# Kernel optimization log

Hardware: AMD Instinct MI355X
Metric: run time of the kernel (lower is better)

Reference implementation:

```python
import jax, jax.numpy as jnp
import numpy as np

V, D, L, H, T, B = 128, 256, 2, 4, 4096, 8
DK, DV = 128, 256           # key_dim=0.5*D, value_dim=1.0*D (fla GLA defaults)
HK, HV = DK // H, DV // H   # 32, 64
GLN = 16.0                  # gate_logit_normalizer
CH = 64                     # chunk size
EPS = 1e-5

def layernorm(x, w, b):
    mu = x.mean(-1, keepdims=True)
    var = ((x - mu) ** 2).mean(-1, keepdims=True)
    return (x - mu) * jax.lax.rsqrt(var + EPS) * w + b

def gla_chunk(q, k, v, gk, scale):
    # q,k,gk: [B,T,H,HK], v: [B,T,H,HV]; gk are per-key log decay gates (<=0)
    B_, T_, H_, dk = q.shape
    dv = v.shape[-1]
    N = T_ // CH
    def rs(x):
        d = x.shape[-1]
        return x.reshape(B_, N, CH, H_, d).transpose(0, 3, 1, 2, 4)  # [B,H,N,C,d]
    q, k, v, gk = rs(q), rs(k), rs(v), rs(gk)
    b = jnp.cumsum(gk, axis=3)                       # inclusive within-chunk cumlog decay
    q_s = q * jnp.exp(b) * scale
    k_i = k * jnp.exp(-b)                            # for intra-chunk attention
    k_e = k * jnp.exp(b[..., -1:, :] - b)            # decayed to chunk end, for state update
    mask = jnp.tril(jnp.ones((CH, CH), bool))
    att = jnp.einsum('bhncd,bhnmd->bhncm', q_s, k_i)
    att = jnp.where(mask, att, 0.0)
    o_intra = jnp.einsum('bhncm,bhnmd->bhncd', att, v)
    g_last = jnp.exp(b[..., -1, :])                  # [B,H,N,dk] full-chunk decay
    kv = jnp.einsum('bhncd,bhnce->bhnde', k_e, v)    # [B,H,N,dk,dv]
    def step(S, inp):
        qc, gl, kvc = inp
        o = jnp.einsum('bhcd,bhde->bhce', qc, S)
        return S * gl[..., None] + kvc, o
    S0 = jnp.zeros((B_, H_, dk, dv), q.dtype)
    xs = (jnp.moveaxis(q_s, 2, 0), jnp.moveaxis(g_last, 2, 0), jnp.moveaxis(kv, 2, 0))
    _, o_inter = jax.lax.scan(step, S0, xs)
    o = o_intra + jnp.moveaxis(o_inter, 0, 2)        # [B,H,N,C,dv]
    return o.transpose(0, 2, 3, 1, 4).reshape(B_, T_, H_, dv)

def gla_attn(x, wq, wk, wv, wg, gk_w1, gk_w2, gk_b2, gnorm_w, wo):
    B_, T_, _ = x.shape
    q = (x @ wq).reshape(B_, T_, H, HK)
    k = (x @ wk).reshape(B_, T_, H, HK)
    v = (x @ wv).reshape(B_, T_, H, HV)
    gk = jax.nn.log_sigmoid(x @ gk_w1 @ gk_w2 + gk_b2) / GLN
    gk = gk.reshape(B_, T_, H, HK)
    o = gla_chunk(q, k, v, gk, HK ** -0.5)           # [B,T,H,HV]
    g = (x @ wg).reshape(B_, T_, H, HV)
    rms = jax.lax.rsqrt((o * o).mean(-1, keepdims=True) + EPS)
    o = o * rms * gnorm_w * (g * jax.nn.sigmoid(g))  # FusedRMSNormSwishGate
    return o.reshape(B_, T_, DV) @ wo

def setup_inputs() -> dict:
    key = jax.random.key(0)
    ks = jax.random.split(key, 16)
    s = 0.02
    return {
        'tokens': jax.random.randint(ks[0], (B, T), 0, V),
        'embed': jax.random.normal(ks[1], (V, D)) * s,
        'ln_w': jnp.ones((L, D)), 'ln_b': jnp.zeros((L, D)),
        'wq': jax.random.normal(ks[2], (L, D, DK)) * s,
        'wk': jax.random.normal(ks[3], (L, D, DK)) * s,
        'wv': jax.random.normal(ks[4], (L, D, DV)) * s,
        'wg': jax.random.normal(ks[5], (L, D, DV)) * s,
        'gk_w1': jax.random.normal(ks[6], (L, D, 16)) * s,
        'gk_w2': jax.random.normal(ks[7], (L, 16, DK)) * s,
        'gk_b2': jnp.zeros((L, DK)),
        'gnorm_w': jnp.ones((L, HV)),
        'wo': jax.random.normal(ks[8], (L, DV, D)) * s,
        'mlp_w1': jax.random.normal(ks[9], (L, D, 2 * D)) * s,
        'mlp_b1': jnp.zeros((L, 2 * D)),
        'mlp_w2': jax.random.normal(ks[10], (L, 2 * D, D)) * s,
        'mlp_b2': jnp.zeros((L, D)),
        'head_w': jax.random.normal(ks[11], (D, V)) * s,
        'head_b': jnp.zeros((V,)),
    }

def reference(tokens, embed, ln_w, ln_b, wq, wk, wv, wg, gk_w1, gk_w2, gk_b2,
              gnorm_w, wo, mlp_w1, mlp_b1, mlp_w2, mlp_b2, head_w, head_b):
    x = embed[tokens]
    for i in range(L):
        h = layernorm(x, ln_w[i], ln_b[i])
        x = x + gla_attn(h, wq[i], wk[i], wv[i], wg[i], gk_w1[i], gk_w2[i],
                         gk_b2[i], gnorm_w[i], wo[i])
        h = layernorm(x, ln_w[i], ln_b[i])
        x = x + jax.nn.gelu(h @ mlp_w1[i] + mlp_b1[i], approximate=False) @ mlp_w2[i] + mlp_b2[i]
    return x @ head_w + head_b
```

## Files before the change

kernel.cpp:

```cpp
#include <hip/hip_runtime.h>
#include <hip/hip_bf16.h>
#include <math.h>

namespace {

constexpr int Bq = 8, Tq = 4096, Dq = 256, Lq = 2, Hq = 4;
constexpr int DKq = 128, DVq = 256, HKq = 32, HVq = 64;
constexpr int Nq = Tq / 64;
constexpr int Mq = Bq * Tq;
constexpr int SQ = 896;
constexpr float SCALEq = 0.17677669529663688f;
constexpr int WL = 1114112;

typedef __hip_bfloat16 bf16;
typedef __attribute__((ext_vector_type(8))) short bf16x8;
typedef __attribute__((ext_vector_type(4))) float f32x4;

__device__ __forceinline__ float b2f(bf16 x) { return __bfloat162float(x); }

__device__ __forceinline__ bf16x8 ld8(const bf16* p) { return *(const bf16x8*)p; }
__device__ __forceinline__ bf16x8 ld8(const float* p) {
  const float4* q4 = (const float4*)p;
  float4 a = q4[0], b = q4[1];
  float v[8] = {a.x, a.y, a.z, a.w, b.x, b.y, b.z, b.w};
  bf16x8 r;
#pragma unroll
  for (int i = 0; i < 8; i++) r[i] = __builtin_bit_cast(short, __float2bfloat16(v[i]));
  return r;
}

__device__ __forceinline__ int swzk(int k, int row) {
  return (k & ~63) | ((((k >> 3) & 7) ^ (row & 7)) << 3) | (k & 7);
}

__device__ __forceinline__ size_t fidx(int n, int k, int K) {
  int ct = n >> 7, nt = (n >> 4) & 7, lr = n & 15;
  int k0 = k >> 6, kk = (k >> 5) & 1, lg = (k >> 3) & 3, e = k & 7;
  int fi = ((ct * (K >> 6) + k0) * 2 + kk) * 8 + nt;
  return (size_t)fi * 512 + (lg * 16 + lr) * 8 + e;
}

__device__ __forceinline__ void wsplit2(float v, bf16* hi, bf16* lo) {
  bf16 h = __float2bfloat16(v);
  *hi = h; *lo = __float2bfloat16(v - b2f(h));
}

__global__ void k_wprep(const float* __restrict__ wq, const float* __restrict__ wk,
                        const float* __restrict__ wv, const float* __restrict__ wg,
                        const float* __restrict__ g1, const float* __restrict__ g2,
                        const float* __restrict__ wo, const float* __restrict__ m1,
                        const float* __restrict__ m2, const float* __restrict__ hw,
                        bf16* __restrict__ Wt) {
  int g = blockIdx.x * 256 + threadIdx.x;
  if (g >= 2 * 540672 + 32768) return;
  if (g < 2 * 540672) {
    int l = g / 540672, r = g % 540672;
    bf16* dst = Wt + (size_t)l * WL;
    if (r < 196608) {
      int k, nf; float v;
      if (r < 32768)       { int r2 = r;          k = r2 >> 7; nf = (r2 & 127);       v = wq[l*32768 + r2]; }
      else if (r < 65536)  { int r2 = r - 32768;  k = r2 >> 7; nf = 128 + (r2 & 127); v = wk[l*32768 + r2]; }
      else if (r < 131072) { int r2 = r - 65536;  k = r2 >> 8; nf = 256 + (r2 & 255); v = wv[l*65536 + r2]; }
      else                 { int r2 = r - 131072; k = r2 >> 8; nf = 512 + (r2 & 255); v = wg[l*65536 + r2]; }
      size_t fo = fidx(nf, k, 256);
      wsplit2(v, &dst[fo], &dst[229376 + fo]);
    } else if (r < 212992) {
      int r2 = r - 196608; int k = r2 >> 7, n = r2 & 127;
      float v = 0.f;
#pragma unroll
      for (int i = 0; i < 16; i++) v += g1[l*4096 + k*16 + i] * g2[l*2048 + i*128 + n];
      size_t fo = fidx(768 + n, k, 256);
      wsplit2(v, &dst[fo], &dst[229376 + fo]);
    } else if (r < 278528) {
      int r2 = r - 212992; int k = r2 >> 8, n = r2 & 255;
      size_t fo = fidx(n, k, 256);
      wsplit2(wo[l*65536 + r2], &dst[458752 + fo], &dst[524288 + fo]);
    } else if (r < 409600) {
      int r2 = r - 278528; int k = r2 >> 9, n = r2 & 511;
      size_t fo = fidx(n, k, 256);
      wsplit2(m1[l*131072 + r2], &dst[589824 + fo], &dst[720896 + fo]);
    } else {
      int r2 = r - 409600; int k = r2 >> 8, n = r2 & 255;
      size_t fo = fidx(n, k, 512);
      wsplit2(m2[l*131072 + r2], &dst[851968 + fo], &dst[983040 + fo]);
    }
  } else {
    int r2 = g - 2 * 540672; int k = r2 >> 7, n = r2 & 127;
    size_t fo = fidx(n, k, 256);
    wsplit2(hw[r2], &Wt[2228224 + fo], &Wt[2228224 + 32768 + fo]);
  }
}

__global__ void k_embed(const int* __restrict__ tok, const float* __restrict__ emb,
                        float* __restrict__ x) {
  int row = blockIdx.x, i = threadIdx.x;
  x[(size_t)row * Dq + i] = emb[(size_t)tok[row] * Dq + i];
}

__global__ void k_ln(const float* __restrict__ x, const float* __restrict__ w,
                     const float* __restrict__ bb, bf16* __restrict__ h) {
  int row = blockIdx.x, i = threadIdx.x;
  float v = x[(size_t)row * Dq + i];
  float s = v, s2 = v * v;
#pragma unroll
  for (int o = 32; o > 0; o >>= 1) { s += __shfl_down(s, o, 64); s2 += __shfl_down(s2, o, 64); }
  __shared__ float rs[4], rs2[4];
  if ((i & 63) == 0) { rs[i >> 6] = s; rs2[i >> 6] = s2; }
  __syncthreads();
  float sum = rs[0] + rs[1] + rs[2] + rs[3];
  float sum2 = rs2[0] + rs2[1] + rs2[2] + rs2[3];
  float mu = sum * (1.f / Dq);
  float var = fmaxf(sum2 * (1.f / Dq) - mu * mu, 0.f);
  float r = rsqrtf(var + 1e-5f);
  h[(size_t)row * Dq + i] = __float2bfloat16((v - mu) * r * w[i] + bb[i]);
}

template <typename AT, typename OT, int EPI, bool BIAS, bool ACC, bool GATEA>
__global__ __launch_bounds__(256, 2) void k_mgemm8(const AT* __restrict__ A, int lda,
                                                   const bf16* __restrict__ Whf,
                                                   const bf16* __restrict__ Wlf,
                                                   const float* __restrict__ bias,
                                                   OT* __restrict__ C, int ldc, int K,
                                                   const bf16* __restrict__ GQ,
                                                   const float* __restrict__ gnw) {
  __shared__ __attribute__((aligned(16))) bf16 At[128 * 256];
  int tid = threadIdx.x;
  int lane = tid & 63, wave = tid >> 6;
  int lr = lane & 15, lg = lane >> 4;
  int wm = (wave >> 1) * 64, wn = (wave & 1) * 64;
  int row0 = blockIdx.x * 128;
  int ct = blockIdx.y, nk = K >> 6;
  f32x4 acc[4][4];
#pragma unroll
  for (int m = 0; m < 4; m++)
#pragma unroll
    for (int n = 0; n < 4; n++) acc[m][n] = (f32x4){0.f, 0.f, 0.f, 0.f};

  for (int kc = 0; kc < K; kc += 256) {
    if (kc) __syncthreads();
#pragma unroll
    for (int p = 0; p < 16; p++) {
      int cix = p * 256 + tid, r = cix >> 5, j = (cix & 31) * 8;
      bf16x8 v = ld8(A + (size_t)(row0 + r) * lda + kc + j);
      if constexpr (GATEA) {
        float o[8]; float s = 0.f;
#pragma unroll
        for (int i = 0; i < 8; i++) { o[i] = b2f(__builtin_bit_cast(bf16, (short)v[i])); s += o[i] * o[i]; }
        s += __shfl_xor(s, 1, 64); s += __shfl_xor(s, 2, 64); s += __shfl_xor(s, 4, 64);
        float rr = rsqrtf(s * (1.f / 64.f) + 1e-5f);
        bf16x8 g8 = *(const bf16x8*)(GQ + (size_t)(row0 + r) * SQ + 512 + j);
#pragma unroll
        for (int i = 0; i < 8; i++) {
          float g = b2f(__builtin_bit_cast(bf16, (short)g8[i]));
          float sw = g / (1.f + expf(-g));
          v[i] = __builtin_bit_cast(short, __float2bfloat16(o[i] * rr * gnw[(j + i) & 63] * sw));
        }
      }
      *(bf16x8*)&At[r * 256 + swzk(j, r)] = v;
    }
    __syncthreads();
#pragma unroll
    for (int k0l = 0; k0l < 256; k0l += 64) {
      int k0 = kc + k0l;
      int k0i = k0 >> 6;
#pragma unroll
      for (int kk = 0; kk < 64; kk += 32) {
        int fb = ((ct * nk + k0i) * 2 + (kk >> 5)) * 8 + (wn >> 4);
        const bf16* bhp = Whf + (size_t)fb * 512 + lane * 8;
        const bf16* blp = Wlf + (size_t)fb * 512 + lane * 8;
        bf16x8 af[4], bh4[4], bl4[4];
#pragma unroll
        for (int n = 0; n < 4; n++) {
          bh4[n] = *(const bf16x8*)(bhp + n * 512);
          bl4[n] = *(const bf16x8*)(blp + n * 512);
        }
#pragma unroll
        for (int m = 0; m < 4; m++) {
          int ar = wm + m * 16 + lr;
          af[m] = *(bf16x8*)&At[ar * 256 + swzk(k0l + kk + lg * 8, ar)];
        }
#pragma unroll
        for (int m = 0; m < 4; m++)
#pragma unroll
          for (int n = 0; n < 4; n++) {
            acc[m][n] = __builtin_amdgcn_mfma_f32_16x16x32_bf16(af[m], bh4[n], acc[m][n], 0, 0, 0);
            acc[m][n] = __builtin_amdgcn_mfma_f32_16x16x32_bf16(af[m], bl4[n], acc[m][n], 0, 0, 0);
          }
      }
    }
  }
#pragma unroll
  for (int m = 0; m < 4; m++) {
#pragma unroll
    for (int n = 0; n < 4; n++) {
      int col = ct * 128 + wn + n * 16 + lr;
      int rowb = row0 + wm + m * 16 + lg * 4;
      float bv = BIAS ? bias[col] : 0.f;
#pragma unroll
      for (int j = 0; j < 4; j++) {
        float v = acc[m][n][j] + bv;
        if (EPI == 2) v = 0.5f * v * (1.f + erff(v * 0.70710678118654752f));
        if (EPI == 3 && col >= 768) {
          float t = v + bias[col - 768];
          v = (fminf(t, 0.f) - log1pf(expf(-fabsf(t)))) * (1.f / 16.f);
        }
        size_t oi = (size_t)(rowb + j) * ldc + col;
        if constexpr (ACC) C[oi] += v;
        else if constexpr (sizeof(OT) == 2) C[oi] = __float2bfloat16(v);
        else C[oi] = v;
      }
    }
  }
}

__global__ __launch_bounds__(256) void k_intra(bf16* QKVG,
                                               bf16* __restrict__ O,
                                               bf16* __restrict__ KVt,
                                               float* __restrict__ GL) {
  int blk = blockIdx.x;
  int n = blk & 63, h = (blk >> 6) & 3, b = blk >> 8;
  __shared__ __attribute__((aligned(16))) char smem[47488];
  float* bshT = (float*)smem;
  bf16*  kvS  = (bf16*)smem;
  float* glv  = (float*)(smem + 8448);
  bf16*  vT   = (bf16*)(smem + 8576);
  bf16*  kiAH = (bf16*)(smem + 17792);
  bf16*  kiAL = (bf16*)(smem + 22400);
  bf16*  qsH  = (bf16*)(smem + 27008);
  bf16*  qsL  = (bf16*)(smem + 32128);
  bf16*  kiBH = (bf16*)(smem + 37248);
  bf16*  kiBL = (bf16*)(smem + 42368);
  bf16*  aH   = (bf16*)(smem + 27008);
  bf16*  aL   = (bf16*)(smem + 36224);
  int tid = threadIdx.x;
  int lane = tid & 63, wave = tid >> 6;
  int lr = lane & 15, lg = lane >> 4;
  size_t tbase = (size_t)b * Tq + n * 64;
  int bh = b * Hq + h;

  {
    int c = tid >> 2, dc = (tid & 3) * 8;
    bf16x8 g8 = *(const bf16x8*)(QKVG + (tbase + c) * SQ + 768 + h * HKq + dc);
#pragma unroll
    for (int i = 0; i < 8; i++) bshT[(dc + i) * 66 + c] = b2f(__builtin_bit_cast(bf16, (short)g8[i]));
  }
  __syncthreads();
#pragma unroll
  for (int dd = 0; dd < 8; dd++) {
    int d = wave * 8 + dd;
    float v = bshT[d * 66 + lane];
#pragma unroll
    for (int o = 1; o < 64; o <<= 1) {
      float t = __shfl_up(v, (unsigned)o, 64);
      if (lane >= o) v += t;
    }
    bshT[d * 66 + lane] = v;
  }
  __syncthreads();
  if (tid < 32) {
    float g = expf(bshT[tid * 66 + 63]);
    glv[tid] = g;
    GL[(size_t)(bh * Nq + n) * 32 + tid] = g;
  }
  {
    int c = tid >> 2, dc = (tid & 3) * 8;
    size_t qoff = (tbase + c) * SQ + h * HKq + dc;
    bf16x8 q8 = *(const bf16x8*)(QKVG + qoff);
    bf16x8 k8 = *(const bf16x8*)(QKVG + qoff + 128);
    bf16x8 qh8, ql8, kh8, kl8;
#pragma unroll
    for (int i = 0; i < 8; i++) {
      float bv = bshT[(dc + i) * 66 + c];
      float qv = b2f(__builtin_bit_cast(bf16, (short)q8[i])) * expf(bv) * SCALEq;
      float kv = b2f(__builtin_bit_cast(bf16, (short)k8[i])) * expf(-bv);
      bf16 qh = __float2bfloat16(qv); bf16 ql = __float2bfloat16(qv - b2f(qh));
      bf16 kh = __float2bfloat16(kv); bf16 kl = __float2bfloat16(kv - b2f(kh));
      qh8[i] = __builtin_bit_cast(short, qh); ql8[i] = __builtin_bit_cast(short, ql);
      kh8[i] = __builtin_bit_cast(short, kh); kl8[i] = __builtin_bit_cast(short, kl);
      kiAH[(dc + i) * 72 + c] = kh; kiAL[(dc + i) * 72 + c] = kl;
    }
    *(bf16x8*)&qsH[c * 40 + dc] = qh8;
    *(bf16x8*)&qsL[c * 40 + dc] = ql8;
    *(bf16x8*)&kiBH[c * 40 + dc] = kh8;
    *(bf16x8*)&kiBL[c * 40 + dc] = kl8;
    *(bf16x8*)(QKVG + qoff) = qh8;
  }
#pragma unroll
  for (int p = 0; p < 2; p++) {
    int idx = p * 256 + tid;
    int c = idx & 63, ec = (idx >> 6) * 8;
    bf16x8 v8 = *(const bf16x8*)(QKVG + (tbase + c) * SQ + 256 + h * HVq + ec);
#pragma unroll
    for (int i = 0; i < 8; i++) vT[(ec + i) * 72 + c] = __builtin_bit_cast(bf16, (short)v8[i]);
  }
  __syncthreads();
  f32x4 accq[4];
#pragma unroll
  for (int t = 0; t < 4; t++) accq[t] = (f32x4){0.f, 0.f, 0.f, 0.f};
  {
    bf16x8 afh = *(bf16x8*)&qsH[(wave * 16 + lr) * 40 + lg * 8];
    bf16x8 afl = *(bf16x8*)&qsL[(wave * 16 + lr) * 40 + lg * 8];
#pragma unroll
    for (int t = 0; t < 4; t++) {
      bf16x8 bh = *(bf16x8*)&kiBH[(t * 16 + lr) * 40 + lg * 8];
      bf16x8 bl = *(bf16x8*)&kiBL[(t * 16 + lr) * 40 + lg * 8];
      accq[t] = __builtin_amdgcn_mfma_f32_16x16x32_bf16(afh, bh, accq[t], 0, 0, 0);
      accq[t] = __builtin_amdgcn_mfma_f32_16x16x32_bf16(afh, bl, accq[t], 0, 0, 0);
      accq[t] = __builtin_amdgcn_mfma_f32_16x16x32_bf16(afl, bh, accq[t], 0, 0, 0);
    }
  }
  __syncthreads();
#pragma unroll
  for (int t = 0; t < 4; t++)
#pragma unroll
    for (int j = 0; j < 4; j++) {
      int row = wave * 16 + lg * 4 + j;
      int col = t * 16 + lr;
      float v = (col <= row) ? accq[t][j] : 0.f;
      bf16 hi = __float2bfloat16(v);
      aH[row * 72 + col] = hi;
      aL[row * 72 + col] = __float2bfloat16(v - b2f(hi));
    }
  __syncthreads();
  f32x4 acco[4];
#pragma unroll
  for (int t = 0; t < 4; t++) acco[t] = (f32x4){0.f, 0.f, 0.f, 0.f};
#pragma unroll
  for (int ks = 0; ks < 2; ks++) {
    bf16x8 ah = *(bf16x8*)&aH[(wave * 16 + lr) * 72 + ks * 32 + lg * 8];
    bf16x8 al = *(bf16x8*)&aL[(wave * 16 + lr) * 72 + ks * 32 + lg * 8];
#pragma unroll
    for (int t = 0; t < 4; t++) {
      bf16x8 bfv = *(bf16x8*)&vT[(t * 16 + lr) * 72 + ks * 32 + lg * 8];
      acco[t] = __builtin_amdgcn_mfma_f32_16x16x32_bf16(ah, bfv, acco[t], 0, 0, 0);
      acco[t] = __builtin_amdgcn_mfma_f32_16x16x32_bf16(al, bfv, acco[t], 0, 0, 0);
    }
  }
#pragma unroll
  for (int t = 0; t < 4; t++)
#pragma unroll
    for (int j = 0; j < 4; j++) {
      int row = wave * 16 + lg * 4 + j, e = t * 16 + lr;
      O[(tbase + row) * DVq + h * HVq + e] = __float2bfloat16(acco[t][j]);
    }
  f32x4 acck[2];
  acck[0] = (f32x4){0.f, 0.f, 0.f, 0.f};
  acck[1] = (f32x4){0.f, 0.f, 0.f, 0.f};
#pragma unroll
  for (int ks = 0; ks < 2; ks++) {
    bf16x8 akh = *(bf16x8*)&kiAH[((wave >> 1) * 16 + lr) * 72 + ks * 32 + lg * 8];
    bf16x8 akl = *(bf16x8*)&kiAL[((wave >> 1) * 16 + lr) * 72 + ks * 32 + lg * 8];
#pragma unroll
    for (int t = 0; t < 2; t++) {
      bf16x8 bfv = *(bf16x8*)&vT[(((wave & 1) * 2 + t) * 16 + lr) * 72 + ks * 32 + lg * 8];
      acck[t] = __builtin_amdgcn_mfma_f32_16x16x32_bf16(akh, bfv, acck[t], 0, 0, 0);
      acck[t] = __builtin_amdgcn_mfma_f32_16x16x32_bf16(akl, bfv, acck[t], 0, 0, 0);
    }
  }
#pragma unroll
  for (int t = 0; t < 2; t++)
#pragma unroll
    for (int j = 0; j < 4; j++) {
      int d = (wave >> 1) * 16 + lg * 4 + j;
      int e = ((wave & 1) * 2 + t) * 16 + lr;
      kvS[d * 72 + e] = __float2bfloat16(acck[t][j] * glv[d]);
    }
  __syncthreads();
  size_t kbase = (size_t)(bh * Nq + n) * 2048;
  {
    int d = tid >> 3, cc = (tid & 7) * 8;
    *(bf16x8*)&KVt[kbase + d * 64 + cc] = *(bf16x8*)&kvS[d * 72 + cc];
  }
}

__global__ __launch_bounds__(256) void k_inter(const bf16* __restrict__ QKVG,
                                               const float* __restrict__ GL,
                                               const bf16* __restrict__ KVt,
                                               bf16* __restrict__ O) {
  int blk = blockIdx.x;
  int es = blk & 7, h = (blk >> 3) & 3, b = blk >> 5;
  int e0 = es * 8;
  __shared__ __attribute__((aligned(16))) bf16 kvl[64 * 32 * 8];
  __shared__ float gl[64 * 32];
  __shared__ float S[64 * 32 * 8];
  int tid = threadIdx.x;
  int bh = b * Hq + h;
  const float* glp = GL + (size_t)bh * Nq * 32;
#pragma unroll
  for (int p = 0; p < 8; p++) { int i = p * 256 + tid; gl[i] = glp[i]; }
  const bf16* kvp = KVt + (size_t)bh * Nq * 2048 + e0;
#pragma unroll
  for (int p = 0; p < 8; p++) {
    int c8 = p * 256 + tid;
    *(bf16x8*)&kvl[c8 * 8] = *(const bf16x8*)(kvp + (size_t)(c8 >> 5) * 2048 + (size_t)(c8 & 31) * 64);
  }
  __syncthreads();
  {
    int pe = tid & 7, pd = tid >> 3;
    float s = 0.f;
    for (int n = 0; n < 64; n++) {
      S[(n * 32 + pd) * 8 + pe] = s;
      s = s * gl[n * 32 + pd] + b2f(kvl[(n * 32 + pd) * 8 + pe]);
    }
  }
  __syncthreads();
  int c = tid >> 2, ep = tid & 3;
  for (int n = 0; n < 64; n++) {
    size_t tbase = (size_t)b * Tq + n * 64;
    const bf16* qp = QKVG + (tbase + c) * SQ + h * HKq;
    const float* Sp = &S[n * 256];
    float a0 = 0.f, a1 = 0.f;
#pragma unroll
    for (int j = 0; j < 4; j++) {
      bf16x8 q8 = *(const bf16x8*)(qp + j * 8);
#pragma unroll
      for (int i = 0; i < 8; i++) {
        float qf = b2f(__builtin_bit_cast(bf16, (short)q8[i]));
        int d = j * 8 + i;
        a0 += qf * Sp[d * 8 + ep];
        a1 += qf * Sp[d * 8 + ep + 4];
      }
    }
    size_t oi = (tbase + c) * DVq + h * HVq + e0 + ep;
    O[oi] = __float2bfloat16(b2f(O[oi]) + a0);
    O[oi + 4] = __float2bfloat16(b2f(O[oi + 4]) + a1);
  }
}

}

extern "C" void kernel_launch(void* const* d_in, const int* in_sizes, int n_in,
                              void* d_out, int out_size, void* d_ws, size_t ws_size,
                              hipStream_t stream) {
  const int*   tok  = (const int*)d_in[0];
  const float* emb  = (const float*)d_in[1];
  const float* ln_w = (const float*)d_in[2];
  const float* ln_b = (const float*)d_in[3];
  const float* wq   = (const float*)d_in[4];
  const float* wk   = (const float*)d_in[5];
  const float* wv   = (const float*)d_in[6];
  const float* wg   = (const float*)d_in[7];
  const float* gkw1 = (const float*)d_in[8];
  const float* gkw2 = (const float*)d_in[9];
  const float* gkb2 = (const float*)d_in[10];
  const float* gnw  = (const float*)d_in[11];
  const float* wo   = (const float*)d_in[12];
  const float* mw1  = (const float*)d_in[13];
  const float* mb1  = (const float*)d_in[14];
  const float* mw2  = (const float*)d_in[15];
  const float* mb2  = (const float*)d_in[16];
  const float* hw   = (const float*)d_in[17];
  const float* hb   = (const float*)d_in[18];

  if (ws_size < 134217728u) return;
  char* w = (char*)d_ws;
  float* X    = (float*)w;
  bf16*  Ob   = (bf16*)(w + 33554432);
  bf16*  Hbf  = Ob;
  bf16*  QKVG = (bf16*)(w + 50331648);
  bf16*  KVt  = (bf16*)(w + 109051904);
  float* GLb  = (float*)(w + 117440512);
  bf16*  Wt   = (bf16*)(w + 117702656);
  bf16*  MLPH = QKVG;

  dim3 blk(256);
  k_wprep<<<4353, blk, 0, stream>>>(wq, wk, wv, wg, gkw1, gkw2, wo, mw1, mw2, hw, Wt);
  k_embed<<<Mq, blk, 0, stream>>>(tok, emb, X);

  for (int l = 0; l < Lq; l++) {
    const bf16* Wl = Wt + (size_t)l * WL;
    k_ln<<<Mq, blk, 0, stream>>>(X, ln_w + l * Dq, ln_b + l * Dq, Hbf);
    k_mgemm8<bf16, bf16, 3, false, false, false><<<dim3(256, 7), blk, 0, stream>>>(Hbf, 256, Wl, Wl + 229376, gkb2 + l * DKq, QKVG, SQ, 256, nullptr, nullptr);
    k_intra<<<Bq * Hq * Nq, blk, 0, stream>>>(QKVG, Ob, KVt, GLb);
    k_inter<<<Bq * Hq * 8, blk, 0, stream>>>(QKVG, GLb, KVt, Ob);
    k_mgemm8<bf16, float, 0, false, true, true><<<dim3(256, 2), blk, 0, stream>>>(Ob, 256, Wl + 458752, Wl + 524288, nullptr, X, 256, 256, QKVG, gnw + l * HVq);
    k_ln<<<Mq, blk, 0, stream>>>(X, ln_w + l * Dq, ln_b + l * Dq, Hbf);
    k_mgemm8<bf16, bf16, 2, true, false, false><<<dim3(256, 4), blk, 0, stream>>>(Hbf, 256, Wl + 589824, Wl + 720896, mb1 + l * 2 * Dq, MLPH, 512, 256, nullptr, nullptr);
    k_mgemm8<bf16, float, 0, true, true, false><<<dim3(256, 2), blk, 0, stream>>>(MLPH, 512, Wl + 851968, Wl + 983040, mb2 + l * Dq, X, 256, 512, nullptr, nullptr);
  }
  k_mgemm8<float, float, 0, true, false, false><<<dim3(256, 1), blk, 0, stream>>>(X, 256, Wt + 2228224, Wt + 2228224 + 32768, hb, (float*)d_out, 128, 256, nullptr, nullptr);
}
```

Baseline: 701.2 us.

## Shrink GEMM A-tile to 64-wide K slices and vectorize layernorm/embed rows

The GEMM now stages A in 64-column K slices instead of 256, cutting shared memory from 64KB to 16KB per block and raising launch bounds to 4 blocks per CU. The cost is an extra barrier per 64-wide slice and less work between barriers. Layernorm and embedding now process 8 rows per block, with each 32-lane group handling one row through float4 loads and bf16x8 stores. This removes the cross-wave shared-memory reduction and lowers the block count.

```diff
diff --git a/kernel.cpp b/kernel.cpp
--- a/kernel.cpp
+++ b/kernel.cpp
@@ -93,37 +93,44 @@
 
 __global__ void k_embed(const int* __restrict__ tok, const float* __restrict__ emb,
                         float* __restrict__ x) {
-  int row = blockIdx.x, i = threadIdx.x;
-  x[(size_t)row * Dq + i] = emb[(size_t)tok[row] * Dq + i];
+  int row = blockIdx.x * 8 + (threadIdx.x >> 5);
+  int j = (threadIdx.x & 31) * 8;
+  const float4* s = (const float4*)(emb + (size_t)tok[row] * Dq + j);
+  float4* d = (float4*)(x + (size_t)row * Dq + j);
+  d[0] = s[0]; d[1] = s[1];
 }
 
 __global__ void k_ln(const float* __restrict__ x, const float* __restrict__ w,
                      const float* __restrict__ bb, bf16* __restrict__ h) {
-  int row = blockIdx.x, i = threadIdx.x;
-  float v = x[(size_t)row * Dq + i];
-  float s = v, s2 = v * v;
-#pragma unroll
-  for (int o = 32; o > 0; o >>= 1) { s += __shfl_down(s, o, 64); s2 += __shfl_down(s2, o, 64); }
-  __shared__ float rs[4], rs2[4];
-  if ((i & 63) == 0) { rs[i >> 6] = s; rs2[i >> 6] = s2; }
-  __syncthreads();
-  float sum = rs[0] + rs[1] + rs[2] + rs[3];
-  float sum2 = rs2[0] + rs2[1] + rs2[2] + rs2[3];
-  float mu = sum * (1.f / Dq);
-  float var = fmaxf(sum2 * (1.f / Dq) - mu * mu, 0.f);
+  int row = blockIdx.x * 8 + (threadIdx.x >> 5);
+  int j = (threadIdx.x & 31) * 8;
+  const float4* xp = (const float4*)(x + (size_t)row * Dq + j);
+  float4 a = xp[0], b4 = xp[1];
+  float v[8] = {a.x, a.y, a.z, a.w, b4.x, b4.y, b4.z, b4.w};
+  float s = 0.f, s2 = 0.f;
+#pragma unroll
+  for (int i = 0; i < 8; i++) { s += v[i]; s2 += v[i] * v[i]; }
+#pragma unroll
+  for (int o = 16; o > 0; o >>= 1) { s += __shfl_xor(s, o, 64); s2 += __shfl_xor(s2, o, 64); }
+  float mu = s * (1.f / Dq);
+  float var = fmaxf(s2 * (1.f / Dq) - mu * mu, 0.f);
   float r = rsqrtf(var + 1e-5f);
-  h[(size_t)row * Dq + i] = __float2bfloat16((v - mu) * r * w[i] + bb[i]);
+  bf16x8 o8;
+#pragma unroll
+  for (int i = 0; i < 8; i++)
+    o8[i] = __builtin_bit_cast(short, __float2bfloat16((v[i] - mu) * r * w[j + i] + bb[j + i]));
+  *(bf16x8*)(h + (size_t)row * Dq + j) = o8;
 }
 
 template <typename AT, typename OT, int EPI, bool BIAS, bool ACC, bool GATEA>
-__global__ __launch_bounds__(256, 2) void k_mgemm8(const AT* __restrict__ A, int lda,
+__global__ __launch_bounds__(256, 4) void k_mgemm7(const AT* __restrict__ A, int lda,
                                                    const bf16* __restrict__ Whf,
                                                    const bf16* __restrict__ Wlf,
                                                    const float* __restrict__ bias,
                                                    OT* __restrict__ C, int ldc, int K,
                                                    const bf16* __restrict__ GQ,
                                                    const float* __restrict__ gnw) {
-  __shared__ __attribute__((aligned(16))) bf16 At[128 * 256];
+  __shared__ __attribute__((aligned(16))) bf16 At[128 * 64];
   int tid = threadIdx.x;
   int lane = tid & 63, wave = tid >> 6;
   int lr = lane & 15, lg = lane >> 4;
@@ -136,58 +143,54 @@
 #pragma unroll
     for (int n = 0; n < 4; n++) acc[m][n] = (f32x4){0.f, 0.f, 0.f, 0.f};
 
-  for (int kc = 0; kc < K; kc += 256) {
-    if (kc) __syncthreads();
-#pragma unroll
-    for (int p = 0; p < 16; p++) {
-      int cix = p * 256 + tid, r = cix >> 5, j = (cix & 31) * 8;
-      bf16x8 v = ld8(A + (size_t)(row0 + r) * lda + kc + j);
+  for (int k0 = 0; k0 < K; k0 += 64) {
+    int k0i = k0 >> 6;
+#pragma unroll
+    for (int p = 0; p < 4; p++) {
+      int cix = p * 256 + tid, r = cix >> 3, j = (cix & 7) * 8;
+      bf16x8 v = ld8(A + (size_t)(row0 + r) * lda + k0 + j);
       if constexpr (GATEA) {
         float o[8]; float s = 0.f;
 #pragma unroll
         for (int i = 0; i < 8; i++) { o[i] = b2f(__builtin_bit_cast(bf16, (short)v[i])); s += o[i] * o[i]; }
         s += __shfl_xor(s, 1, 64); s += __shfl_xor(s, 2, 64); s += __shfl_xor(s, 4, 64);
         float rr = rsqrtf(s * (1.f / 64.f) + 1e-5f);
-        bf16x8 g8 = *(const bf16x8*)(GQ + (size_t)(row0 + r) * SQ + 512 + j);
+        bf16x8 g8 = *(const bf16x8*)(GQ + (size_t)(row0 + r) * SQ + 512 + k0 + j);
 #pragma unroll
         for (int i = 0; i < 8; i++) {
           float g = b2f(__builtin_bit_cast(bf16, (short)g8[i]));
           float sw = g / (1.f + expf(-g));
-          v[i] = __builtin_bit_cast(short, __float2bfloat16(o[i] * rr * gnw[(j + i) & 63] * sw));
+          v[i] = __builtin_bit_cast(short, __float2bfloat16(o[i] * rr * gnw[(k0 + j + i) & 63] * sw));
         }
       }
-      *(bf16x8*)&At[r * 256 + swzk(j, r)] = v;
+      *(bf16x8*)&At[r * 64 + swzk(j, r)] = v;
     }
     __syncthreads();
 #pragma unroll
-    for (int k0l = 0; k0l < 256; k0l += 64) {
-      int k0 = kc + k0l;
-      int k0i = k0 >> 6;
-#pragma unroll
-      for (int kk = 0; kk < 64; kk += 32) {
-        int fb = ((ct * nk + k0i) * 2 + (kk >> 5)) * 8 + (wn >> 4);
-        const bf16* bhp = Whf + (size_t)fb * 512 + lane * 8;
-        const bf16* blp = Wlf + (size_t)fb * 512 + lane * 8;
-        bf16x8 af[4], bh4[4], bl4[4];
+    for (int kk = 0; kk < 64; kk += 32) {
+      int fb = ((ct * nk + k0i) * 2 + (kk >> 5)) * 8 + (wn >> 4);
+      const bf16* bhp = Whf + (size_t)fb * 512 + lane * 8;
+      const bf16* blp = Wlf + (size_t)fb * 512 + lane * 8;
+      bf16x8 af[4], bh4[4], bl4[4];
+#pragma unroll
+      for (int n = 0; n < 4; n++) {
+        bh4[n] = *(const bf16x8*)(bhp + n * 512);
+        bl4[n] = *(const bf16x8*)(blp + n * 512);
+      }
+#pragma unroll
+      for (int m = 0; m < 4; m++) {
+        int ar = wm + m * 16 + lr;
+        af[m] = *(bf16x8*)&At[ar * 64 + swzk(kk + lg * 8, ar)];
+      }
+#pragma unroll
+      for (int m = 0; m < 4; m++)
 #pragma unroll
         for (int n = 0; n < 4; n++) {
-          bh4[n] = *(const bf16x8*)(bhp + n * 512);
-          bl4[n] = *(const bf16x8*)(blp + n * 512);
+          acc[m][n] = __builtin_amdgcn_mfma_f32_16x16x32_bf16(af[m], bh4[n], acc[m][n], 0, 0, 0);
+          acc[m][n] = __builtin_amdgcn_mfma_f32_16x16x32_bf16(af[m], bl4[n], acc[m][n], 0, 0, 0);
         }
-#pragma unroll
-        for (int m = 0; m < 4; m++) {
-          int ar = wm + m * 16 + lr;
-          af[m] = *(bf16x8*)&At[ar * 256 + swzk(k0l + kk + lg * 8, ar)];
-        }
-#pragma unroll
-        for (int m = 0; m < 4; m++)
-#pragma unroll
-          for (int n = 0; n < 4; n++) {
-            acc[m][n] = __builtin_amdgcn_mfma_f32_16x16x32_bf16(af[m], bh4[n], acc[m][n], 0, 0, 0);
-            acc[m][n] = __builtin_amdgcn_mfma_f32_16x16x32_bf16(af[m], bl4[n], acc[m][n], 0, 0, 0);
-          }
-      }
-    }
+    }
+    __syncthreads();
   }
 #pragma unroll
   for (int m = 0; m < 4; m++) {
@@ -465,18 +468,18 @@
 
   dim3 blk(256);
   k_wprep<<<4353, blk, 0, stream>>>(wq, wk, wv, wg, gkw1, gkw2, wo, mw1, mw2, hw, Wt);
-  k_embed<<<Mq, blk, 0, stream>>>(tok, emb, X);
+  k_embed<<<Mq / 8, blk, 0, stream>>>(tok, emb, X);
 
   for (int l = 0; l < Lq; l++) {
     const bf16* Wl = Wt + (size_t)l * WL;
-    k_ln<<<Mq, blk, 0, stream>>>(X, ln_w + l * Dq, ln_b + l * Dq, Hbf);
-    k_mgemm8<bf16, bf16, 3, false, false, false><<<dim3(256, 7), blk, 0, stream>>>(Hbf, 256, Wl, Wl + 229376, gkb2 + l * DKq, QKVG, SQ, 256, nullptr, nullptr);
+    k_ln<<<Mq / 8, blk, 0, stream>>>(X, ln_w + l * Dq, ln_b + l * Dq, Hbf);
+    k_mgemm7<bf16, bf16, 3, false, false, false><<<dim3(256, 7), blk, 0, stream>>>(Hbf, 256, Wl, Wl + 229376, gkb2 + l * DKq, QKVG, SQ, 256, nullptr, nullptr);
     k_intra<<<Bq * Hq * Nq, blk, 0, stream>>>(QKVG, Ob, KVt, GLb);
     k_inter<<<Bq * Hq * 8, blk, 0, stream>>>(QKVG, GLb, KVt, Ob);
-    k_mgemm8<bf16, float, 0, false, true, true><<<dim3(256, 2), blk, 0, stream>>>(Ob, 256, Wl + 458752, Wl + 524288, nullptr, X, 256, 256, QKVG, gnw + l * HVq);
-    k_ln<<<Mq, blk, 0, stream>>>(X, ln_w + l * Dq, ln_b + l * Dq, Hbf);
-    k_mgemm8<bf16, bf16, 2, true, false, false><<<dim3(256, 4), blk, 0, stream>>>(Hbf, 256, Wl + 589824, Wl + 720896, mb1 + l * 2 * Dq, MLPH, 512, 256, nullptr, nullptr);
-    k_mgemm8<bf16, float, 0, true, true, false><<<dim3(256, 2), blk, 0, stream>>>(MLPH, 512, Wl + 851968, Wl + 983040, mb2 + l * Dq, X, 256, 512, nullptr, nullptr);
-  }
-  k_mgemm8<float, float, 0, true, false, false><<<dim3(256, 1), blk, 0, stream>>>(X, 256, Wt + 2228224, Wt + 2228224 + 32768, hb, (float*)d_out, 128, 256, nullptr, nullptr);
-}
+    k_mgemm7<bf16, float, 0, false, true, true><<<dim3(256, 2), blk, 0, stream>>>(Ob, 256, Wl + 458752, Wl + 524288, nullptr, X, 256, 256, QKVG, gnw + l * HVq);
+    k_ln<<<Mq / 8, blk, 0, stream>>>(X, ln_w + l * Dq, ln_b + l * Dq, Hbf);
+    k_mgemm7<bf16, bf16, 2, true, false, false><<<dim3(256, 4), blk, 0, stream>>>(Hbf, 256, Wl + 589824, Wl + 720896, mb1 + l * 2 * Dq, MLPH, 512, 256, nullptr, nullptr);
+    k_mgemm7<bf16, float, 0, true, true, false><<<dim3(256, 2), blk, 0, stream>>>(MLPH, 512, Wl + 851968, Wl + 983040, mb2 + l * Dq, X, 256, 512, nullptr, nullptr);
+  }
+  k_mgemm7<float, float, 0, true, false, false><<<dim3(256, 1), blk, 0, stream>>>(X, 256, Wt + 2228224, Wt + 2228224 + 32768, hb, (float*)d_out, 128, 256, nullptr, nullptr);
+}
```

After: 643.8 us. 8.2% less time.
